# Kernel optimization log

Hardware: AMD Instinct MI355X
Metric: run time of the kernel (lower is better)

Reference implementation:

```python
import jax, jax.numpy as jnp
import numpy as np

SCALES = (3, 5, 7)

def _avg_pool3d_same(x, k):
    # stride-1 avg_pool3d with padding k//2, count_include_pad=True (torch default).
    # For odd k <= dim this preserves the spatial size, so the subsequent
    # F.interpolate to the input size is an exact identity.
    p = k // 2
    s = jax.lax.reduce_window(
        x, 0.0, jax.lax.add,
        window_dimensions=(1, 1, k, k, k),
        window_strides=(1, 1, 1, 1, 1),
        padding=[(0, 0), (0, 0), (p, p), (p, p), (p, p)])
    return s * (1.0 / float(k ** 3))

def setup_inputs() -> dict:
    key = jax.random.key(0)
    k1, k2 = jax.random.split(key)
    B, C, D, H, W = 2, 48, 64, 64, 64
    x = jax.random.normal(k1, (B, C, D, H, W), dtype=jnp.float32)
    fuse_w = jax.random.normal(k2, (1, len(SCALES) * C), dtype=jnp.float32) * 0.05
    fuse_b = jnp.zeros((1,), dtype=jnp.float32)
    return {"x": x, "fuse_w": fuse_w, "fuse_b": fuse_b}

def reference(x, fuse_w, fuse_b):
    # Multi-scale stride-1 average pooling (sizes preserved -> interp is identity)
    pooled = [_avg_pool3d_same(x, k) for k in SCALES]   # each (B, C, D, H, W)
    cat = jnp.concatenate(pooled, axis=1)               # (B, 3C, D, H, W)
    # 1x1x1 conv to a single channel, then sigmoid
    out = jnp.einsum('bcdhw,oc->bodhw', cat, fuse_w) + fuse_b[None, :, None, None, None]
    return jax.nn.sigmoid(out)                          # (B, 1, D, H, W)
```

## Files before the change

### kernel.cpp

```cpp
#include <hip/hip_runtime.h>
#include <math.h>

#define CH       48
#define DIM      64
#define SPATIAL  (DIM * DIM * DIM)
#define NB       2
#define VOL      (NB * SPATIAL)
#define NS       3
#define ROWS     16

typedef float f4 __attribute__((ext_vector_type(4)));

__global__ __launch_bounds__(256) void k_chanred_wpool(
        const float* __restrict__ x,
        const float* __restrict__ fw,
        float* __restrict__ z) {
    __shared__ float sw[NS * CH];
    __shared__ f4 tile[NS][ROWS][16];
    const int tid = threadIdx.x;
    if (tid < NS * CH) sw[tid] = fw[tid];
    __syncthreads();

    const int lr  = tid >> 4;
    const int lw  = tid & 15;
    const int row = blockIdx.x * ROWS + lr;
    const int b   = row >> 12;

    const f4* xp = (const f4*)x
        + (size_t)b * CH * (SPATIAL / 4)
        + (size_t)(row & 4095) * 16 + lw;

    f4 a0 = {0,0,0,0}, a1 = {0,0,0,0}, a2 = {0,0,0,0};
    #pragma unroll 8
    for (int c = 0; c < CH; ++c) {
        f4 v = __builtin_nontemporal_load(&xp[(size_t)c * (SPATIAL / 4)]);
        a0 += sw[c] * v;
        a1 += sw[CH + c] * v;
        a2 += sw[2 * CH + c] * v;
    }
    tile[0][lr][lw] = a0;
    tile[1][lr][lw] = a1;
    tile[2][lr][lw] = a2;
    __syncthreads();

    f4* z4 = (f4*)z;
    const size_t ob = (size_t)row * 16 + lw;
    const f4 zero = {0,0,0,0};
    #pragma unroll
    for (int s = 0; s < NS; ++s) {
        f4 m1 = (lw > 0)  ? tile[s][lr][lw - 1] : zero;
        f4 m0 = tile[s][lr][lw];
        f4 p1 = (lw < 15) ? tile[s][lr][lw + 1] : zero;
        float f[12] = {m1.x, m1.y, m1.z, m1.w,
                       m0.x, m0.y, m0.z, m0.w,
                       p1.x, p1.y, p1.z, p1.w};
        const int p = s + 1;
        f4 r;
        #pragma unroll
        for (int j = 0; j < 4; ++j) {
            float acc = 0.f;
            #pragma unroll
            for (int i = -3; i <= 3; ++i)
                if (i >= -p && i <= p) acc += f[4 + j + i];
            r[j] = acc;
        }
        z4[(size_t)s * (VOL / 4) + ob] = r;
    }
}

__global__ __launch_bounds__(256) void k_poolh(
        const float* __restrict__ in, float* __restrict__ out) {
    int gid = blockIdx.x * blockDim.x + threadIdx.x;
    int s   = gid >> 17;
    int r   = gid & 0x1FFFF;
    int h   = (r >> 4) & 63;
    int p   = s + 1;
    const f4* col = (const f4*)in + ((size_t)s << 17) + (r - (h << 4));
    int lo = h - p; if (lo < 0)  lo = 0;
    int hi = h + p; if (hi > 63) hi = 63;
    f4 a = {0,0,0,0};
    for (int hh = lo; hh <= hi; ++hh) a += col[hh << 4];
    ((f4*)out)[gid] = a;
}

__global__ __launch_bounds__(256) void k_poold_fuse(
        const float* __restrict__ in,
        const float* __restrict__ fb,
        float* __restrict__ out) {
    int gid = blockIdx.x * blockDim.x + threadIdx.x;
    int d   = (gid >> 10) & 63;
    int base = gid - (d << 10);
    const float inv[NS] = {1.f / 27.f, 1.f / 125.f, 1.f / 343.f};
    const float bias = fb[0];
    f4 acc = {bias, bias, bias, bias};
    #pragma unroll
    for (int s = 0; s < NS; ++s) {
        int p  = s + 1;
        int lo = d - p; if (lo < 0)  lo = 0;
        int hi = d + p; if (hi > 63) hi = 63;
        const f4* bp = (const f4*)in + ((size_t)s << 17) + base;
        f4 a = {0,0,0,0};
        for (int dd = lo; dd <= hi; ++dd) a += bp[dd << 10];
        acc += a * inv[s];
    }
    f4 r;
    #pragma unroll
    for (int j = 0; j < 4; ++j) r[j] = 1.f / (1.f + __expf(-acc[j]));
    __builtin_nontemporal_store(r, &((f4*)out)[gid]);
}

extern "C" void kernel_launch(void* const* d_in, const int* in_sizes, int n_in,
                              void* d_out, int out_size, void* d_ws, size_t ws_size,
                              hipStream_t stream) {
    const float* x  = (const float*)d_in[0];
    const float* fw = (const float*)d_in[1];
    const float* fb = (const float*)d_in[2];
    float* out = (float*)d_out;

    float* ws0 = (float*)d_ws;
    float* ws1 = ws0 + (size_t)NS * VOL;

    k_chanred_wpool<<<(NB * DIM * DIM) / ROWS, 256, 0, stream>>>(x, fw, ws0);
    k_poolh<<<(NS * VOL / 4) / 256, 256, 0, stream>>>(ws0, ws1);
    k_poold_fuse<<<(VOL / 4) / 256, 256, 0, stream>>>(ws1, fb, out);
}
```

Before: 32.84 us.

## Fuse H and D pooling into one LDS-tiled kernel with transposed intermediate

The first kernel now writes its channel-reduced, W-pooled result in a transposed layout: one plane per (scale, batch, w-quad), indexed by (d,h). The separate H-pool and D-pool+sigmoid kernels are merged into one kernel. Each block loads a D-slab with a halo of 3 planes for all three scales into shared memory, pools along H in place, then pools along D and applies the sigmoid. This removes one launch and the round trip through a second workspace buffer. The cost is halo re-reads, a large shared-memory footprint limiting occupancy, only 256 blocks, and output stores strided by w4.

```diff
diff --git a/kernel.cpp b/kernel.cpp
--- a/kernel.cpp
+++ b/kernel.cpp
@@ -8,13 +8,16 @@
 #define VOL      (NB * SPATIAL)
 #define NS       3
 #define ROWS     16
+#define ZT_PLANE 4096
+#define DT       8
+#define DTH      (DT + 6)
 
 typedef float f4 __attribute__((ext_vector_type(4)));
 
-__global__ __launch_bounds__(256) void k_chanred_wpool(
+__global__ __launch_bounds__(256) void kA(
         const float* __restrict__ x,
         const float* __restrict__ fw,
-        float* __restrict__ z) {
+        float* __restrict__ zt) {
     __shared__ float sw[NS * CH];
     __shared__ f4 tile[NS][ROWS][16];
     const int tid = threadIdx.x;
@@ -25,10 +28,11 @@
     const int lw  = tid & 15;
     const int row = blockIdx.x * ROWS + lr;
     const int b   = row >> 12;
+    const int dh  = row & 4095;
 
     const f4* xp = (const f4*)x
         + (size_t)b * CH * (SPATIAL / 4)
-        + (size_t)(row & 4095) * 16 + lw;
+        + (size_t)dh * 16 + lw;
 
     f4 a0 = {0,0,0,0}, a1 = {0,0,0,0}, a2 = {0,0,0,0};
     #pragma unroll 8
@@ -43,8 +47,7 @@
     tile[2][lr][lw] = a2;
     __syncthreads();
 
-    f4* z4 = (f4*)z;
-    const size_t ob = (size_t)row * 16 + lw;
+    f4* zt4 = (f4*)zt;
     const f4 zero = {0,0,0,0};
     #pragma unroll
     for (int s = 0; s < NS; ++s) {
@@ -64,49 +67,90 @@
                 if (i >= -p && i <= p) acc += f[4 + j + i];
             r[j] = acc;
         }
-        z4[(size_t)s * (VOL / 4) + ob] = r;
+        zt4[((size_t)(s * NB + b) * 16 + lw) * ZT_PLANE + dh] = r;
     }
 }
 
-__global__ __launch_bounds__(256) void k_poolh(
-        const float* __restrict__ in, float* __restrict__ out) {
-    int gid = blockIdx.x * blockDim.x + threadIdx.x;
-    int s   = gid >> 17;
-    int r   = gid & 0x1FFFF;
-    int h   = (r >> 4) & 63;
-    int p   = s + 1;
-    const f4* col = (const f4*)in + ((size_t)s << 17) + (r - (h << 4));
-    int lo = h - p; if (lo < 0)  lo = 0;
-    int hi = h + p; if (hi > 63) hi = 63;
-    f4 a = {0,0,0,0};
-    for (int hh = lo; hh <= hi; ++hh) a += col[hh << 4];
-    ((f4*)out)[gid] = a;
-}
-
-__global__ __launch_bounds__(256) void k_poold_fuse(
-        const float* __restrict__ in,
+__global__ __launch_bounds__(256) void kB(
+        const float* __restrict__ zt,
         const float* __restrict__ fb,
         float* __restrict__ out) {
-    int gid = blockIdx.x * blockDim.x + threadIdx.x;
-    int d   = (gid >> 10) & 63;
-    int base = gid - (d << 10);
+    __shared__ f4 tile[NS][DTH][DIM];
+    const int tid = threadIdx.x;
+    const int bid = blockIdx.x;
+    const int w4  = bid & 15;
+    const int d0  = ((bid >> 4) & 7) * DT;
+    const int b   = bid >> 7;
+
+    const f4* zt4 = (const f4*)zt;
+    #pragma unroll
+    for (int s = 0; s < NS; ++s) {
+        const f4* src = zt4 + ((size_t)(s * NB + b) * 16 + w4) * ZT_PLANE;
+        #pragma unroll
+        for (int t = 0; t < (DTH * DIM + 255) / 256; ++t) {
+            int i = tid + t * 256;
+            if (i < DTH * DIM) {
+                int dd = i >> 6, h = i & 63;
+                int gd = d0 - 3 + dd;
+                f4 v = {0,0,0,0};
+                if (gd >= 0 && gd < DIM) v = src[gd * 64 + h];
+                tile[s][dd][h] = v;
+            }
+        }
+    }
+    __syncthreads();
+
+    const int NITEM = NS * DTH * DIM;
+    f4 acc[11];
+    #pragma unroll
+    for (int t = 0; t < 11; ++t) {
+        int j = tid + t * 256;
+        f4 a = {0,0,0,0};
+        if (j < NITEM) {
+            int s   = j / (DTH * DIM);
+            int rem = j - s * (DTH * DIM);
+            int dd  = rem >> 6, h = rem & 63;
+            int p   = s + 1;
+            int lo  = h - p; if (lo < 0)  lo = 0;
+            int hi  = h + p; if (hi > 63) hi = 63;
+            for (int hh = lo; hh <= hi; ++hh) a += tile[s][dd][hh];
+        }
+        acc[t] = a;
+    }
+    __syncthreads();
+    #pragma unroll
+    for (int t = 0; t < 11; ++t) {
+        int j = tid + t * 256;
+        if (j < NITEM) {
+            int s   = j / (DTH * DIM);
+            int rem = j - s * (DTH * DIM);
+            tile[s][rem >> 6][rem & 63] = acc[t];
+        }
+    }
+    __syncthreads();
+
     const float inv[NS] = {1.f / 27.f, 1.f / 125.f, 1.f / 343.f};
     const float bias = fb[0];
-    f4 acc = {bias, bias, bias, bias};
+    f4* out4 = (f4*)out;
     #pragma unroll
-    for (int s = 0; s < NS; ++s) {
-        int p  = s + 1;
-        int lo = d - p; if (lo < 0)  lo = 0;
-        int hi = d + p; if (hi > 63) hi = 63;
-        const f4* bp = (const f4*)in + ((size_t)s << 17) + base;
-        f4 a = {0,0,0,0};
-        for (int dd = lo; dd <= hi; ++dd) a += bp[dd << 10];
-        acc += a * inv[s];
+    for (int t = 0; t < DT * DIM / 256; ++t) {
+        int j   = tid + t * 256;
+        int ddp = j >> 6, h = j & 63;
+        int d   = d0 + ddp;
+        f4 a2 = {bias, bias, bias, bias};
+        #pragma unroll
+        for (int s = 0; s < NS; ++s) {
+            int p = s + 1;
+            f4 a = {0,0,0,0};
+            for (int i = -3; i <= 3; ++i)
+                if (i >= -p && i <= p) a += tile[s][ddp + 3 + i][h];
+            a2 += a * inv[s];
+        }
+        f4 r;
+        #pragma unroll
+        for (int jj = 0; jj < 4; ++jj) r[jj] = 1.f / (1.f + __expf(-a2[jj]));
+        out4[(size_t)b * (SPATIAL / 4) + (size_t)d * 1024 + h * 16 + w4] = r;
     }
-    f4 r;
-    #pragma unroll
-    for (int j = 0; j < 4; ++j) r[j] = 1.f / (1.f + __expf(-acc[j]));
-    __builtin_nontemporal_store(r, &((f4*)out)[gid]);
 }
 
 extern "C" void kernel_launch(void* const* d_in, const int* in_sizes, int n_in,
@@ -117,10 +161,8 @@
     const float* fb = (const float*)d_in[2];
     float* out = (float*)d_out;
 
-    float* ws0 = (float*)d_ws;
-    float* ws1 = ws0 + (size_t)NS * VOL;
+    float* zt = (float*)d_ws;
 
-    k_chanred_wpool<<<(NB * DIM * DIM) / ROWS, 256, 0, stream>>>(x, fw, ws0);
-    k_poolh<<<(NS * VOL / 4) / 256, 256, 0, stream>>>(ws0, ws1);
-    k_poold_fuse<<<(VOL / 4) / 256, 256, 0, stream>>>(ws1, fb, out);
+    kA<<<(NB * DIM * DIM * DIM / ROWS) / 64, 256, 0, stream>>>(x, fw, zt);
+    kB<<<NB * 16 * (DIM / DT), 256, 0, stream>>>(zt, fb, out);
 }
```

Measured after the change: 31.56 us. 3.9% less time.

## Fuse H-axis pooling into channel-reduction kernel using full-plane tiles

Applied to the files above, without the earlier changes.

Each block now processes an entire 64x64 (b,d) plane, reducing the 48 channels to three weighted maps and then applying both the W and H box sums in shared memory. This removes the separate H-pooling kernel along with its intermediate buffer round trip and launch. The cost is that the grid shrinks to 128 blocks, which may underuse the GPU's compute units during the bandwidth-heavy read of x, and the shared-memory tile becomes larger.

```diff
diff --git a/kernel.cpp b/kernel.cpp
--- a/kernel.cpp
+++ b/kernel.cpp
@@ -7,105 +7,136 @@
 #define NB       2
 #define VOL      (NB * SPATIAL)
 #define NS       3
-#define ROWS     16
+#define CSTRIDE  (DIM * 1024)
 
 typedef float f4 __attribute__((ext_vector_type(4)));
 
-__global__ __launch_bounds__(256) void k_chanred_wpool(
+__global__ __launch_bounds__(256) void kA(
         const float* __restrict__ x,
         const float* __restrict__ fw,
         float* __restrict__ z) {
     __shared__ float sw[NS * CH];
-    __shared__ f4 tile[NS][ROWS][16];
+    __shared__ f4 tile[NS][DIM][16];
     const int tid = threadIdx.x;
     if (tid < NS * CH) sw[tid] = fw[tid];
     __syncthreads();
 
-    const int lr  = tid >> 4;
-    const int lw  = tid & 15;
-    const int row = blockIdx.x * ROWS + lr;
-    const int b   = row >> 12;
+    const int bd = blockIdx.x;
+    const int b  = bd >> 6;
+    const int w4 = tid & 15;
+    const int r0 = tid >> 4;
 
     const f4* xp = (const f4*)x
-        + (size_t)b * CH * (SPATIAL / 4)
-        + (size_t)(row & 4095) * 16 + lw;
+        + ((size_t)b * CH * DIM + (bd & 63)) * 1024 + r0 * 16 + w4;
 
-    f4 a0 = {0,0,0,0}, a1 = {0,0,0,0}, a2 = {0,0,0,0};
-    #pragma unroll 8
+    f4 acc[NS][4];
+    #pragma unroll
+    for (int s = 0; s < NS; ++s)
+        #pragma unroll
+        for (int rp = 0; rp < 4; ++rp) acc[s][rp] = (f4){0,0,0,0};
+
+    #pragma unroll 4
     for (int c = 0; c < CH; ++c) {
-        f4 v = __builtin_nontemporal_load(&xp[(size_t)c * (SPATIAL / 4)]);
-        a0 += sw[c] * v;
-        a1 += sw[CH + c] * v;
-        a2 += sw[2 * CH + c] * v;
+        const f4* cp = xp + (size_t)c * CSTRIDE;
+        f4 v0 = __builtin_nontemporal_load(cp);
+        f4 v1 = __builtin_nontemporal_load(cp + 256);
+        f4 v2 = __builtin_nontemporal_load(cp + 512);
+        f4 v3 = __builtin_nontemporal_load(cp + 768);
+        float s0 = sw[c], s1 = sw[CH + c], s2 = sw[2 * CH + c];
+        acc[0][0] += s0 * v0; acc[0][1] += s0 * v1; acc[0][2] += s0 * v2; acc[0][3] += s0 * v3;
+        acc[1][0] += s1 * v0; acc[1][1] += s1 * v1; acc[1][2] += s1 * v2; acc[1][3] += s1 * v3;
+        acc[2][0] += s2 * v0; acc[2][1] += s2 * v1; acc[2][2] += s2 * v2; acc[2][3] += s2 * v3;
     }
-    tile[0][lr][lw] = a0;
-    tile[1][lr][lw] = a1;
-    tile[2][lr][lw] = a2;
+
+    #pragma unroll
+    for (int s = 0; s < NS; ++s)
+        #pragma unroll
+        for (int rp = 0; rp < 4; ++rp)
+            tile[s][r0 + 16 * rp][w4] = acc[s][rp];
     __syncthreads();
 
-    f4* z4 = (f4*)z;
-    const size_t ob = (size_t)row * 16 + lw;
     const f4 zero = {0,0,0,0};
     #pragma unroll
     for (int s = 0; s < NS; ++s) {
-        f4 m1 = (lw > 0)  ? tile[s][lr][lw - 1] : zero;
-        f4 m0 = tile[s][lr][lw];
-        f4 p1 = (lw < 15) ? tile[s][lr][lw + 1] : zero;
-        float f[12] = {m1.x, m1.y, m1.z, m1.w,
-                       m0.x, m0.y, m0.z, m0.w,
-                       p1.x, p1.y, p1.z, p1.w};
         const int p = s + 1;
-        f4 r;
         #pragma unroll
-        for (int j = 0; j < 4; ++j) {
-            float acc = 0.f;
+        for (int rp = 0; rp < 4; ++rp) {
+            const int r = r0 + 16 * rp;
+            f4 m1 = (w4 > 0)  ? tile[s][r][w4 - 1] : zero;
+            f4 m0 = acc[s][rp];
+            f4 p1 = (w4 < 15) ? tile[s][r][w4 + 1] : zero;
+            float f[12] = {m1.x, m1.y, m1.z, m1.w,
+                           m0.x, m0.y, m0.z, m0.w,
+                           p1.x, p1.y, p1.z, p1.w};
+            f4 r4;
             #pragma unroll
-            for (int i = -3; i <= 3; ++i)
-                if (i >= -p && i <= p) acc += f[4 + j + i];
-            r[j] = acc;
+            for (int j = 0; j < 4; ++j) {
+                float a = 0.f;
+                #pragma unroll
+                for (int i = -3; i <= 3; ++i)
+                    if (i >= -p && i <= p) a += f[4 + j + i];
+                r4[j] = a;
+            }
+            acc[s][rp] = r4;
         }
-        z4[(size_t)s * (VOL / 4) + ob] = r;
+    }
+    __syncthreads();
+
+    #pragma unroll
+    for (int s = 0; s < NS; ++s)
+        #pragma unroll
+        for (int rp = 0; rp < 4; ++rp)
+            tile[s][r0 + 16 * rp][w4] = acc[s][rp];
+    __syncthreads();
+
+    f4* zp = (f4*)z + (size_t)bd * 1024 + w4;
+    #pragma unroll
+    for (int s = 0; s < NS; ++s) {
+        const int p = s + 1;
+        #pragma unroll
+        for (int rp = 0; rp < 4; ++rp) {
+            const int r = r0 + 16 * rp;
+            f4 a = {0,0,0,0};
+            #pragma unroll
+            for (int i = -3; i <= 3; ++i) {
+                const int rr = r + i;
+                if (i >= -p && i <= p && rr >= 0 && rr < DIM)
+                    a += tile[s][rr][w4];
+            }
+            zp[(size_t)s * (NB * DIM * 1024) + r * 16] = a;
+        }
     }
 }
 
-__global__ __launch_bounds__(256) void k_poolh(
-        const float* __restrict__ in, float* __restrict__ out) {
-    int gid = blockIdx.x * blockDim.x + threadIdx.x;
-    int s   = gid >> 17;
-    int r   = gid & 0x1FFFF;
-    int h   = (r >> 4) & 63;
-    int p   = s + 1;
-    const f4* col = (const f4*)in + ((size_t)s << 17) + (r - (h << 4));
-    int lo = h - p; if (lo < 0)  lo = 0;
-    int hi = h + p; if (hi > 63) hi = 63;
-    f4 a = {0,0,0,0};
-    for (int hh = lo; hh <= hi; ++hh) a += col[hh << 4];
-    ((f4*)out)[gid] = a;
-}
-
-__global__ __launch_bounds__(256) void k_poold_fuse(
-        const float* __restrict__ in,
+__global__ __launch_bounds__(256) void kB(
+        const float* __restrict__ z,
         const float* __restrict__ fb,
         float* __restrict__ out) {
-    int gid = blockIdx.x * blockDim.x + threadIdx.x;
-    int d   = (gid >> 10) & 63;
-    int base = gid - (d << 10);
+    const int gid = blockIdx.x * 256 + threadIdx.x;
+    const int pl  = gid & 1023;
+    const int d   = (gid >> 10) & 63;
+    const int b   = gid >> 16;
+
+    const f4* z4 = (const f4*)z;
     const float inv[NS] = {1.f / 27.f, 1.f / 125.f, 1.f / 343.f};
     const float bias = fb[0];
-    f4 acc = {bias, bias, bias, bias};
+    f4 a2 = {bias, bias, bias, bias};
     #pragma unroll
     for (int s = 0; s < NS; ++s) {
-        int p  = s + 1;
-        int lo = d - p; if (lo < 0)  lo = 0;
-        int hi = d + p; if (hi > 63) hi = 63;
-        const f4* bp = (const f4*)in + ((size_t)s << 17) + base;
+        const int p = s + 1;
+        const size_t base = ((size_t)s * NB * DIM + b * DIM) * 1024 + pl;
         f4 a = {0,0,0,0};
-        for (int dd = lo; dd <= hi; ++dd) a += bp[dd << 10];
-        acc += a * inv[s];
+        #pragma unroll
+        for (int i = -3; i <= 3; ++i) {
+            const int dd = d + i;
+            if (i >= -p && i <= p && dd >= 0 && dd < DIM)
+                a += z4[base + (size_t)dd * 1024];
+        }
+        a2 += a * inv[s];
     }
     f4 r;
     #pragma unroll
-    for (int j = 0; j < 4; ++j) r[j] = 1.f / (1.f + __expf(-acc[j]));
+    for (int j = 0; j < 4; ++j) r[j] = 1.f / (1.f + __expf(-a2[j]));
     __builtin_nontemporal_store(r, &((f4*)out)[gid]);
 }
 
@@ -117,10 +148,8 @@
     const float* fb = (const float*)d_in[2];
     float* out = (float*)d_out;
 
-    float* ws0 = (float*)d_ws;
-    float* ws1 = ws0 + (size_t)NS * VOL;
+    float* z = (float*)d_ws;
 
-    k_chanred_wpool<<<(NB * DIM * DIM) / ROWS, 256, 0, stream>>>(x, fw, ws0);
-    k_poolh<<<(NS * VOL / 4) / 256, 256, 0, stream>>>(ws0, ws1);
-    k_poold_fuse<<<(VOL / 4) / 256, 256, 0, stream>>>(ws1, fb, out);
+    kA<<<NB * DIM, 256, 0, stream>>>(x, fw, z);
+    kB<<<(VOL / 4) / 256, 256, 0, stream>>>(z, fb, out);
 }
```

New measurement: 36.68 us. 1.12x slower.
